# Kernel tuning notes

Hardware: AMD Instinct MI355X
Metric: run time of the kernel (lower is better)

## Reference

```python
import jax, jax.numpy as jnp
import numpy as np

HIDDEN = 4544
NUM_HEADS = 71
HEAD_DIM = 64
ROPE_BASE = 10000.0


def _rope_cos_sin(seq_len, dim, dtype):
    inv_freq = 1.0 / (ROPE_BASE ** (jnp.arange(0, dim, 2, dtype=jnp.float32) / dim))
    t = jnp.arange(seq_len, dtype=jnp.float32)
    freqs = jnp.einsum('i,j->ij', t, inv_freq)            # [S, dim/2]
    emb = jnp.concatenate([freqs, freqs], axis=-1)        # [S, dim]
    return jnp.cos(emb).astype(dtype), jnp.sin(emb).astype(dtype)


def _rotate_half(x):
    half = x.shape[-1] // 2
    return jnp.concatenate([-x[..., half:], x[..., :half]], axis=-1)


def _apply_rope(x, cos, sin):
    # x: [..., S, hd]; cos/sin: [S, hd]
    return x * cos + _rotate_half(x) * sin


def setup_inputs() -> dict:
    key = jax.random.key(0)
    k1, k2, k3 = jax.random.split(key, 3)
    B, S = 1, 1024
    hidden_states = jax.random.normal(k1, (B, 1, S, HIDDEN), dtype=jnp.float32) * 0.02
    # additive causal mask (prefill)
    neg = jnp.triu(jnp.full((S, S), -1e9, dtype=jnp.float32), k=1)
    attention_mask = jnp.broadcast_to(neg[None, None], (B, 1, S, S))
    # fused QKV weight (already transposed for right-matmul): [H, (nh+2)*hd]
    qkv_w = jax.random.normal(k2, (HIDDEN, (NUM_HEADS + 2) * HEAD_DIM), dtype=jnp.float32) * 0.02
    dense_w = jax.random.normal(k3, (HIDDEN, HIDDEN), dtype=jnp.float32) * 0.02
    return {"hidden_states": hidden_states, "attention_mask": attention_mask,
            "qkv_w": qkv_w, "dense_w": dense_w}


def reference(hidden_states, attention_mask, qkv_w, dense_w):
    B, _, S, H = hidden_states.shape
    nh, hd = NUM_HEADS, HEAD_DIM
    x = hidden_states[:, 0]                               # [B, S, H]
    fused = jnp.einsum('bsh,hf->bsf', x, qkv_w)           # [B, S, (nh+2)*hd]
    fused = fused.reshape(B, S, nh + 2, hd)
    q = jnp.transpose(fused[:, :, :nh, :], (0, 2, 1, 3))  # [B, nh, S, hd]
    k = fused[:, :, nh, :]                                # [B, S, hd]  (single KV head, MQA)
    v = fused[:, :, nh + 1, :]                            # [B, S, hd]
    cos, sin = _rope_cos_sin(S, hd, q.dtype)
    q = _apply_rope(q, cos, sin)
    k = _apply_rope(k, cos, sin)
    scale = 1.0 / np.sqrt(hd).astype(np.float32)
    scores = jnp.einsum('bhsd,btd->bhst', q, k) * scale   # [B, nh, S, S]
    scores = scores + attention_mask                      # broadcast over heads
    probs = jax.nn.softmax(scores, axis=-1)
    ctx = jnp.einsum('bhst,btd->bhsd', probs, v)          # [B, nh, S, hd]
    ctx = jnp.transpose(ctx, (0, 2, 1, 3)).reshape(B, S, nh * hd)
    out = jnp.einsum('bsh,hg->bsg', ctx, dense_w)         # [B, S, H]
    return out[:, None]                                   # [B, 1, S, H]
```

## Files before the change

kernel.cpp:

```cpp
#include <hip/hip_runtime.h>

#define S_LEN 1024
#define HID   4544
#define NH    71
#define NQKV  4672

typedef __attribute__((ext_vector_type(4))) float f32x4;
typedef __attribute__((ext_vector_type(4))) unsigned short u16x4;
typedef __attribute__((ext_vector_type(8))) unsigned short u16x8;
typedef __attribute__((ext_vector_type(8))) __bf16 bf16x8;

__device__ __forceinline__ bf16x8 as_bf(u16x8 v) { return __builtin_bit_cast(bf16x8, v); }

__device__ __forceinline__ unsigned short f2bf(float f) {
    unsigned u = __builtin_bit_cast(unsigned, f);
    return (unsigned short)((u + 0x7FFFu + ((u >> 16) & 1u)) >> 16);
}
__device__ __forceinline__ float bf2f(unsigned short u) {
    return __builtin_bit_cast(float, (unsigned)u << 16);
}
__device__ __forceinline__ unsigned pk2(float a, float b) {
    return (unsigned)f2bf(a) | ((unsigned)f2bf(b) << 16);
}
__device__ __forceinline__ void gload16(const void* g, void* l) {
    __builtin_amdgcn_global_load_lds((const __attribute__((address_space(1))) unsigned int*)g,
                                     (__attribute__((address_space(3))) unsigned int*)l,
                                     16, 0, 0);
}

__global__ __launch_bounds__(256) void cvt_x_kernel(const float4* __restrict__ x,
                                                    ushort4* __restrict__ y) {
    int i = blockIdx.x * 256 + threadIdx.x;
    float4 v = x[i];
    ushort4 r;
    r.x = f2bf(v.x); r.y = f2bf(v.y); r.z = f2bf(v.z); r.w = f2bf(v.w);
    y[i] = r;
}

__global__ __launch_bounds__(256) void cvt_wT_kernel(const float* __restrict__ w,
                                                     unsigned short* __restrict__ wt,
                                                     int K, int N) {
    __shared__ float t[64][65];
    int n0 = blockIdx.x * 64, k0 = blockIdx.y * 64;
    int tx = threadIdx.x & 15, ty = threadIdx.x >> 4;
#pragma unroll
    for (int r = 0; r < 64; r += 16) {
        int k = k0 + ty + r;
        float4 v = *(const float4*)&w[(size_t)k * N + n0 + tx * 4];
        t[ty + r][tx * 4 + 0] = v.x;
        t[ty + r][tx * 4 + 1] = v.y;
        t[ty + r][tx * 4 + 2] = v.z;
        t[ty + r][tx * 4 + 3] = v.w;
    }
    __syncthreads();
    int nr = threadIdx.x >> 2;
    int kq = (threadIdx.x & 3) * 16;
    unsigned short tmp[16];
#pragma unroll
    for (int z = 0; z < 16; z++) tmp[z] = f2bf(t[kq + z][nr]);
    u16x8* dst = (u16x8*)&wt[(size_t)(n0 + nr) * K + k0 + kq];
    dst[0] = *(const u16x8*)&tmp[0];
    dst[1] = *(const u16x8*)&tmp[8];
}

__global__ void rope_table_kernel(float* __restrict__ cs, float* __restrict__ sn) {
    int s = blockIdx.x, i = threadIdx.x;
    float inv = powf(10000.0f, -(2.0f * (float)i) / 64.0f);
    float f = (float)s * inv;
    cs[s * 32 + i] = cosf(f);
    sn[s * 32 + i] = sinf(f);
}

template<int EPI>
__global__ __launch_bounds__(256, 3) void gemm_bt_kernel(
        const unsigned short* __restrict__ A, const unsigned short* __restrict__ BT,
        void* __restrict__ Cout, const float* __restrict__ cs_t,
        const float* __restrict__ sn_t, unsigned short* __restrict__ k_out,
        unsigned short* __restrict__ v_out, int K, int ldc) {
    __shared__ unsigned short As[2][128 * 64];
    __shared__ unsigned short Bs[2][64 * 64];
    int p = blockIdx.x;
    int per = gridDim.x >> 3;
    int l = (p & 7) * per + (p >> 3);
    int m0 = (l & 7) * 128, ni_b = l >> 3, n0 = ni_b * 64;
    int t = threadIdx.x;
    int wv = t >> 6, lane = t & 63, lr = lane & 15, lg = lane >> 4;
    int mw = wv * 32;
    int sw = lr & 7;
    int srow = t >> 3, sc16 = t & 7;

    f32x4 acc[2][4];
#pragma unroll
    for (int mi = 0; mi < 2; mi++)
#pragma unroll
        for (int ni = 0; ni < 4; ni++) acc[mi][ni] = (f32x4)0.0f;

    const char* Ab = (const char*)A;
    const char* Bb = (const char*)BT;
    size_t rs = (size_t)K * 2;

    auto stage = [&](int step, int buf) {
        size_t kb = (size_t)step * 128;
#pragma unroll
        for (int i = 0; i < 4; i++) {
            int row = i * 32 + srow;
            int csrc = sc16 ^ (row & 7);
            gload16(Ab + (size_t)(m0 + row) * rs + kb + csrc * 16,
                    (char*)As[buf] + (i * 256 + t) * 16);
        }
#pragma unroll
        for (int i = 0; i < 2; i++) {
            int row = i * 32 + srow;
            int csrc = sc16 ^ (row & 7);
            gload16(Bb + (size_t)(n0 + row) * rs + kb + csrc * 16,
                    (char*)Bs[buf] + (i * 256 + t) * 16);
        }
    };

    int nsteps = K >> 6;
    stage(0, 0);
    if (nsteps > 1) stage(1, 1);
    for (int s = 0; s < nsteps; ++s) {
        int cur = s & 1;
        if (s + 1 < nsteps) { asm volatile("s_waitcnt vmcnt(4)" ::: "memory"); }
        else                { asm volatile("s_waitcnt vmcnt(0)" ::: "memory"); }
        __builtin_amdgcn_s_barrier();
        bf16x8 af[2][2], bfr[4][2];
#pragma unroll
        for (int mi = 0; mi < 2; mi++)
#pragma unroll
            for (int kk = 0; kk < 2; kk++) {
                int row = mw + mi * 16 + lr;
                af[mi][kk] = as_bf(*(const u16x8*)&As[cur][row * 64 + (((kk * 4 + lg) ^ sw) << 3)]);
            }
#pragma unroll
        for (int ni = 0; ni < 4; ni++)
#pragma unroll
            for (int kk = 0; kk < 2; kk++) {
                int row = ni * 16 + lr;
                bfr[ni][kk] = as_bf(*(const u16x8*)&Bs[cur][row * 64 + (((kk * 4 + lg) ^ sw) << 3)]);
            }
#pragma unroll
        for (int mi = 0; mi < 2; mi++)
#pragma unroll
            for (int ni = 0; ni < 4; ni++) {
                acc[mi][ni] = __builtin_amdgcn_mfma_f32_16x16x32_bf16(af[mi][0], bfr[ni][0], acc[mi][ni], 0, 0, 0);
                acc[mi][ni] = __builtin_amdgcn_mfma_f32_16x16x32_bf16(af[mi][1], bfr[ni][1], acc[mi][ni], 0, 0, 0);
            }
        __builtin_amdgcn_s_barrier();
        if (s + 2 < nsteps) stage(s + 2, cur);
    }

    if (EPI == 0) {
        float* C = (float*)Cout;
#pragma unroll
        for (int mi = 0; mi < 2; mi++)
#pragma unroll
            for (int ni = 0; ni < 4; ni++) {
                int col = n0 + ni * 16 + lr;
#pragma unroll
                for (int i = 0; i < 4; i++) {
                    int row = m0 + mw + mi * 16 + 4 * lg + i;
                    C[(size_t)row * ldc + col] = acc[mi][ni][i];
                }
            }
    } else {
        int hh = ni_b;
        if (hh == 72) {
#pragma unroll
            for (int mi = 0; mi < 2; mi++)
#pragma unroll
                for (int ni = 0; ni < 4; ni++) {
                    int d = ni * 16 + lr;
                    int s0 = m0 + mw + mi * 16 + 4 * lg;
                    u16x4 pk;
#pragma unroll
                    for (int i = 0; i < 4; i++) pk[i] = f2bf(acc[mi][ni][i]);
                    *(u16x4*)&v_out[(size_t)d * S_LEN + s0] = pk;
                }
        } else {
            unsigned short* qb = (unsigned short*)Cout;
            float qscale = (hh < 71) ? 0.125f : 1.0f;
#pragma unroll
            for (int mi = 0; mi < 2; mi++)
#pragma unroll
                for (int i = 0; i < 4; i++) {
                    int s = m0 + mw + mi * 16 + 4 * lg + i;
                    float c0 = cs_t[s * 32 + lr],      g0 = sn_t[s * 32 + lr];
                    float c1 = cs_t[s * 32 + 16 + lr], g1 = sn_t[s * 32 + 16 + lr];
#pragma unroll
                    for (int ni = 0; ni < 4; ni++) {
                        float x  = acc[mi][ni][i];
                        float xp = acc[mi][ni ^ 2][i];
                        float c = (ni & 1) ? c1 : c0;
                        float g = (ni & 1) ? g1 : g0;
                        float r = (ni < 2) ? (x * c - xp * g) : (x * c + xp * g);
                        r *= qscale;
                        int d = ni * 16 + lr;
                        if (hh < 71) qb[(size_t)s * HID + hh * 64 + d] = f2bf(r);
                        else         k_out[(size_t)s * 64 + d] = f2bf(r);
                    }
                }
        }
    }
}

__global__ __launch_bounds__(256, 3) void attn_kernel(
        const unsigned short* __restrict__ qb, const unsigned short* __restrict__ kr,
        const unsigned short* __restrict__ vt, unsigned short* __restrict__ ctx,
        unsigned short* __restrict__ Opart, float2* __restrict__ MLpart) {
    __shared__ unsigned short Ks[2][64 * 64];
    __shared__ unsigned short Vs[2][64 * 64];
    __shared__ unsigned short Pl[4][16 * 72];
    int h = blockIdx.y;
    int u = blockIdx.x;
    int c, j0;
    if (u < 16)      { c = 0; j0 = u * 4; }
    else if (u < 28) { c = 1; j0 = 16 + (u - 16) * 4; }
    else if (u < 36) { c = 2; j0 = 32 + (u - 28) * 4; }
    else             { c = 3; j0 = 48 + (u - 36) * 4; }
    int t = threadIdx.x, wv = t >> 6, lane = t & 63, lr = lane & 15, lg = lane >> 4;
    int j = j0 + wv;
    int qs = j * 16 + lr;
    int k_lo = c * 256;
    int kend_w   = min((j + 1) * 16, k_lo + 256);
    int kend_max = min((j0 + 4) * 16, k_lo + 256);
    int nt = (kend_max - k_lo) >> 6;
    int nch = (j >> 4) + 1;
    int srow = t >> 3, sc16 = t & 7, sw = lr & 7;

    auto stage = [&](int ti, int buf) {
        size_t kbase = (size_t)(k_lo + ti * 64);
#pragma unroll
        for (int i = 0; i < 2; i++) {
            int row = i * 32 + srow;
            int csrc = sc16 ^ (row & 7);
            gload16((const char*)kr + (kbase + row) * 128 + csrc * 16,
                    (char*)Ks[buf] + (i * 256 + t) * 16);
        }
#pragma unroll
        for (int i = 0; i < 2; i++) {
            int row = i * 32 + srow;
            int csrc = sc16 ^ (row & 7);
            gload16((const char*)vt + (size_t)row * 2048 + kbase * 2 + csrc * 16,
                    (char*)Vs[buf] + (i * 256 + t) * 16);
        }
    };

    bf16x8 qf[2];
#pragma unroll
    for (int dc = 0; dc < 2; dc++)
        qf[dc] = as_bf(*(const u16x8*)&qb[(size_t)qs * HID + h * 64 + dc * 32 + 8 * lg]);

    float m_i = -1e30f, l_i = 0.0f;
    f32x4 o[4];
#pragma unroll
    for (int d4 = 0; d4 < 4; d4++) o[d4] = (f32x4)0.0f;

    stage(0, 0);
    if (nt > 1) stage(1, 1);

    for (int ti = 0; ti < nt; ti++) {
        int cur = ti & 1;
        if (ti + 1 < nt) { asm volatile("s_waitcnt vmcnt(4)" ::: "memory"); }
        else             { asm volatile("s_waitcnt vmcnt(0)" ::: "memory"); }
        __builtin_amdgcn_s_barrier();
        int k0 = k_lo + ti * 64;
        if (k0 < kend_w) {
            f32x4 st[4];
#pragma unroll
            for (int nc = 0; nc < 4; nc++) st[nc] = (f32x4)0.0f;
#pragma unroll
            for (int nc = 0; nc < 4; nc++) {
                int krow = nc * 16 + lr;
#pragma unroll
                for (int dc = 0; dc < 2; dc++) {
                    bf16x8 kf = as_bf(*(const u16x8*)&Ks[cur][krow * 64 + (((dc * 4 + lg) ^ sw) << 3)]);
                    st[nc] = __builtin_amdgcn_mfma_f32_16x16x32_bf16(kf, qf[dc], st[nc], 0, 0, 0);
                }
            }
            bool needmask = (k0 + 64 > j * 16);
            float mx = -1e30f;
            if (needmask) {
#pragma unroll
                for (int nc = 0; nc < 4; nc++)
#pragma unroll
                    for (int i = 0; i < 4; i++) {
                        int ks = k0 + nc * 16 + 4 * lg + i;
                        float v = (ks <= qs) ? st[nc][i] : -1e30f;
                        st[nc][i] = v;
                        mx = fmaxf(mx, v);
                    }
            } else {
#pragma unroll
                for (int nc = 0; nc < 4; nc++)
#pragma unroll
                    for (int i = 0; i < 4; i++) mx = fmaxf(mx, st[nc][i]);
            }
            mx = fmaxf(mx, __shfl_xor(mx, 16));
            mx = fmaxf(mx, __shfl_xor(mx, 32));
            if (!__all(mx <= m_i + 8.0f)) {
                float mn = fmaxf(m_i, mx);
                float so = __expf(m_i - mn);
                l_i *= so;
#pragma unroll
                for (int d4 = 0; d4 < 4; d4++)
#pragma unroll
                    for (int i = 0; i < 4; i++) o[d4][i] *= so;
                m_i = mn;
            }
            float ps = 0.0f;
#pragma unroll
            for (int nc = 0; nc < 4; nc++)
#pragma unroll
                for (int i = 0; i < 4; i++) {
                    float v = st[nc][i];
                    float e = (!needmask || v > -1e29f) ? __expf(v - m_i) : 0.0f;
                    st[nc][i] = e;
                    ps += e;
                }
            ps += __shfl_xor(ps, 16);
            ps += __shfl_xor(ps, 32);
            l_i += ps;
#pragma unroll
            for (int nc = 0; nc < 4; nc++) {
                *(unsigned*)&Pl[wv][lr * 72 + nc * 16 + 4 * lg]     = pk2(st[nc][0], st[nc][1]);
                *(unsigned*)&Pl[wv][lr * 72 + nc * 16 + 4 * lg + 2] = pk2(st[nc][2], st[nc][3]);
            }
            bf16x8 pb[2];
#pragma unroll
            for (int kk = 0; kk < 2; kk++)
                pb[kk] = as_bf(*(const u16x8*)&Pl[wv][lr * 72 + kk * 32 + 8 * lg]);
#pragma unroll
            for (int d4 = 0; d4 < 4; d4++) {
                int vrow = d4 * 16 + lr;
#pragma unroll
                for (int kk = 0; kk < 2; kk++) {
                    bf16x8 vf = as_bf(*(const u16x8*)&Vs[cur][vrow * 64 + (((kk * 4 + lg) ^ sw) << 3)]);
                    o[d4] = __builtin_amdgcn_mfma_f32_16x16x32_bf16(vf, pb[kk], o[d4], 0, 0, 0);
                }
            }
        }
        __builtin_amdgcn_s_barrier();
        if (ti + 2 < nt) stage(ti + 2, cur);
    }

    if (nch == 1) {
        float linv = 1.0f / l_i;
#pragma unroll
        for (int d4 = 0; d4 < 4; d4++) {
            u16x4 pk;
#pragma unroll
            for (int i = 0; i < 4; i++) pk[i] = f2bf(o[d4][i] * linv);
            *(u16x4*)&ctx[(size_t)qs * HID + h * 64 + d4 * 16 + 4 * lg] = pk;
        }
    } else {
        int pi = (h * 48 + (j - 16)) * 4 + c;
#pragma unroll
        for (int d4 = 0; d4 < 4; d4++) {
            u16x4 pk;
#pragma unroll
            for (int i = 0; i < 4; i++) pk[i] = f2bf(o[d4][i]);
            *(u16x4*)&Opart[(size_t)pi * 1024 + lr * 64 + d4 * 16 + 4 * lg] = pk;
        }
        if (lg == 0) MLpart[pi * 16 + lr] = make_float2(m_i, l_i);
    }
}

__global__ __launch_bounds__(256) void merge_kernel(
        const unsigned short* __restrict__ Opart, const float2* __restrict__ MLpart,
        unsigned short* __restrict__ ctx) {
    int mu = blockIdx.x * 4 + (threadIdx.x >> 6);
    int lane = threadIdx.x & 63;
    int h = mu / 48, jj = mu % 48, j = 16 + jj;
    int nch = (j >> 4) + 1;
    int base = (h * 48 + jj) * 4;
    for (int q = 0; q < 16; q++) {
        float m[4], l[4], w[4];
        float M = -1e30f;
        for (int c = 0; c < nch; c++) {
            float2 ml = MLpart[(base + c) * 16 + q];
            m[c] = ml.x; l[c] = ml.y;
            M = fmaxf(M, m[c]);
        }
        float L = 0.0f;
        for (int c = 0; c < nch; c++) { w[c] = __expf(m[c] - M); L += l[c] * w[c]; }
        float acc = 0.0f;
        for (int c = 0; c < nch; c++)
            acc += w[c] * bf2f(Opart[(size_t)(base + c) * 1024 + q * 64 + lane]);
        ctx[(size_t)(j * 16 + q) * HID + h * 64 + lane] = f2bf(acc / L);
    }
}

extern "C" void kernel_launch(void* const* d_in, const int* in_sizes, int n_in,
                              void* d_out, int out_size, void* d_ws, size_t ws_size,
                              hipStream_t stream) {
    const float* hs      = (const float*)d_in[0];
    const float* qkv_w   = (const float*)d_in[2];
    const float* dense_w = (const float*)d_in[3];
    float* out = (float*)d_out;

    char* ws = (char*)d_ws;
    size_t off = 0;
    auto alloc = [&](size_t bytes) -> void* {
        void* p = ws + off;
        off += (bytes + 255) & ~(size_t)255;
        return p;
    };
    unsigned short* x_bf   = (unsigned short*)alloc((size_t)S_LEN * HID * 2);
    unsigned short* wqkvT  = (unsigned short*)alloc((size_t)NQKV * HID * 2);
    unsigned short* q_bf   = (unsigned short*)alloc((size_t)S_LEN * HID * 2);
    unsigned short* k_rope = (unsigned short*)alloc((size_t)S_LEN * 64 * 2);
    unsigned short* v_t    = (unsigned short*)alloc((size_t)64 * S_LEN * 2);
    unsigned short* ctx    = (unsigned short*)alloc((size_t)S_LEN * HID * 2);
    unsigned short* wdT    = (unsigned short*)alloc((size_t)HID * HID * 2);
    float*          cs_t   = (float*)alloc((size_t)S_LEN * 32 * 4);
    float*          sn_t   = (float*)alloc((size_t)S_LEN * 32 * 4);
    (void)ws_size;
    unsigned short* Opart  = wqkvT;
    float2*         MLpart = (float2*)((char*)wqkvT + (size_t)71 * 48 * 4 * 1024 * 2);

    cvt_x_kernel<<<dim3(S_LEN * HID / 1024), dim3(256), 0, stream>>>(
        (const float4*)hs, (ushort4*)x_bf);
    cvt_wT_kernel<<<dim3(NQKV / 64, HID / 64), dim3(256), 0, stream>>>(
        qkv_w, wqkvT, HID, NQKV);
    cvt_wT_kernel<<<dim3(HID / 64, HID / 64), dim3(256), 0, stream>>>(
        dense_w, wdT, HID, HID);
    rope_table_kernel<<<dim3(S_LEN), dim3(32), 0, stream>>>(cs_t, sn_t);

    gemm_bt_kernel<1><<<dim3(NQKV / 64 * 8), dim3(256), 0, stream>>>(
        x_bf, wqkvT, q_bf, cs_t, sn_t, k_rope, v_t, HID, HID);

    attn_kernel<<<dim3(40, NH), dim3(256), 0, stream>>>(
        q_bf, k_rope, v_t, ctx, Opart, MLpart);

    merge_kernel<<<dim3(NH * 48 / 4), dim3(256), 0, stream>>>(Opart, MLpart, ctx);

    gemm_bt_kernel<0><<<dim3(HID / 64 * 8), dim3(256), 0, stream>>>(
        ctx, wdT, out, nullptr, nullptr, nullptr, nullptr, HID, HID);
}
```

Before: 251.5 us.

## Switch GEMM to 32x32x16 MFMA with two-wave 64x64 warp tiles

The bf16 GEMM kernel moves from 4 waves with 32x64 per-wave tiles of 16x16x32 MFMAs to 2 waves (128 threads), each computing a 64x64 tile with 32x32x16 MFMAs. LDS fragments are read into registers before the second barrier so the next stage's global-to-LDS prefetch can be issued ahead of the MFMA loop. The epilogues, including fused RoPE and V transpose, are remapped to the 32x32 accumulator layout. This aims for fewer LDS reads per FLOP and better MFMA throughput, at the cost of fewer waves per block, higher register pressure and less latency hiding.

```diff
diff --git a/kernel.cpp b/kernel.cpp
--- a/kernel.cpp
+++ b/kernel.cpp
@@ -5,7 +5,8 @@
 #define NH    71
 #define NQKV  4672
 
-typedef __attribute__((ext_vector_type(4))) float f32x4;
+typedef __attribute__((ext_vector_type(4)))  float f32x4;
+typedef __attribute__((ext_vector_type(16))) float f32x16;
 typedef __attribute__((ext_vector_type(4))) unsigned short u16x4;
 typedef __attribute__((ext_vector_type(8))) unsigned short u16x8;
 typedef __attribute__((ext_vector_type(8))) __bf16 bf16x8;
@@ -72,7 +73,7 @@
 }
 
 template<int EPI>
-__global__ __launch_bounds__(256, 3) void gemm_bt_kernel(
+__global__ __launch_bounds__(128, 2) void gemm_bt_kernel(
         const unsigned short* __restrict__ A, const unsigned short* __restrict__ BT,
         void* __restrict__ Cout, const float* __restrict__ cs_t,
         const float* __restrict__ sn_t, unsigned short* __restrict__ k_out,
@@ -84,16 +85,16 @@
     int l = (p & 7) * per + (p >> 3);
     int m0 = (l & 7) * 128, ni_b = l >> 3, n0 = ni_b * 64;
     int t = threadIdx.x;
-    int wv = t >> 6, lane = t & 63, lr = lane & 15, lg = lane >> 4;
-    int mw = wv * 32;
-    int sw = lr & 7;
-    int srow = t >> 3, sc16 = t & 7;
-
-    f32x4 acc[2][4];
+    int wv = t >> 6, lane = t & 63;
+    int lrow = lane & 31;
+    int lk   = lane >> 5;
+    int mw = wv * 64;
+
+    f32x16 acc[2][2];
 #pragma unroll
     for (int mi = 0; mi < 2; mi++)
 #pragma unroll
-        for (int ni = 0; ni < 4; ni++) acc[mi][ni] = (f32x4)0.0f;
+        for (int ni = 0; ni < 2; ni++) acc[mi][ni] = (f32x16)0.0f;
 
     const char* Ab = (const char*)A;
     const char* Bb = (const char*)BT;
@@ -102,18 +103,20 @@
     auto stage = [&](int step, int buf) {
         size_t kb = (size_t)step * 128;
 #pragma unroll
+        for (int i = 0; i < 8; i++) {
+            int chunk = i * 128 + t;
+            int row = chunk >> 3, c16 = chunk & 7;
+            int csrc = c16 ^ (row & 7);
+            gload16(Ab + (size_t)(m0 + row) * rs + kb + csrc * 16,
+                    (char*)As[buf] + chunk * 16);
+        }
+#pragma unroll
         for (int i = 0; i < 4; i++) {
-            int row = i * 32 + srow;
-            int csrc = sc16 ^ (row & 7);
-            gload16(Ab + (size_t)(m0 + row) * rs + kb + csrc * 16,
-                    (char*)As[buf] + (i * 256 + t) * 16);
-        }
-#pragma unroll
-        for (int i = 0; i < 2; i++) {
-            int row = i * 32 + srow;
-            int csrc = sc16 ^ (row & 7);
+            int chunk = i * 128 + t;
+            int row = chunk >> 3, c16 = chunk & 7;
+            int csrc = c16 ^ (row & 7);
             gload16(Bb + (size_t)(n0 + row) * rs + kb + csrc * 16,
-                    (char*)Bs[buf] + (i * 256 + t) * 16);
+                    (char*)Bs[buf] + chunk * 16);
         }
     };
 
@@ -122,33 +125,35 @@
     if (nsteps > 1) stage(1, 1);
     for (int s = 0; s < nsteps; ++s) {
         int cur = s & 1;
-        if (s + 1 < nsteps) { asm volatile("s_waitcnt vmcnt(4)" ::: "memory"); }
+        if (s + 1 < nsteps) { asm volatile("s_waitcnt vmcnt(12)" ::: "memory"); }
         else                { asm volatile("s_waitcnt vmcnt(0)" ::: "memory"); }
         __builtin_amdgcn_s_barrier();
-        bf16x8 af[2][2], bfr[4][2];
-#pragma unroll
-        for (int mi = 0; mi < 2; mi++)
-#pragma unroll
-            for (int kk = 0; kk < 2; kk++) {
-                int row = mw + mi * 16 + lr;
-                af[mi][kk] = as_bf(*(const u16x8*)&As[cur][row * 64 + (((kk * 4 + lg) ^ sw) << 3)]);
-            }
-#pragma unroll
-        for (int ni = 0; ni < 4; ni++)
-#pragma unroll
-            for (int kk = 0; kk < 2; kk++) {
-                int row = ni * 16 + lr;
-                bfr[ni][kk] = as_bf(*(const u16x8*)&Bs[cur][row * 64 + (((kk * 4 + lg) ^ sw) << 3)]);
-            }
-#pragma unroll
-        for (int mi = 0; mi < 2; mi++)
-#pragma unroll
-            for (int ni = 0; ni < 4; ni++) {
-                acc[mi][ni] = __builtin_amdgcn_mfma_f32_16x16x32_bf16(af[mi][0], bfr[ni][0], acc[mi][ni], 0, 0, 0);
-                acc[mi][ni] = __builtin_amdgcn_mfma_f32_16x16x32_bf16(af[mi][1], bfr[ni][1], acc[mi][ni], 0, 0, 0);
-            }
+        bf16x8 af[2][4], bfr[2][4];
+#pragma unroll
+        for (int mi = 0; mi < 2; mi++) {
+            int row = mw + mi * 32 + lrow;
+#pragma unroll
+            for (int kk = 0; kk < 4; kk++)
+                af[mi][kk] = as_bf(*(const u16x8*)&As[cur][row * 64 + (((kk * 2 + lk) ^ (row & 7)) << 3)]);
+        }
+#pragma unroll
+        for (int ni = 0; ni < 2; ni++) {
+            int row = ni * 32 + lrow;
+#pragma unroll
+            for (int kk = 0; kk < 4; kk++)
+                bfr[ni][kk] = as_bf(*(const u16x8*)&Bs[cur][row * 64 + (((kk * 2 + lk) ^ (row & 7)) << 3)]);
+        }
+        asm volatile("s_waitcnt lgkmcnt(0)" ::: "memory");
         __builtin_amdgcn_s_barrier();
         if (s + 2 < nsteps) stage(s + 2, cur);
+#pragma unroll
+        for (int kk = 0; kk < 4; kk++)
+#pragma unroll
+            for (int mi = 0; mi < 2; mi++)
+#pragma unroll
+                for (int ni = 0; ni < 2; ni++)
+                    acc[mi][ni] = __builtin_amdgcn_mfma_f32_32x32x16_bf16(
+                        af[mi][kk], bfr[ni][kk], acc[mi][ni], 0, 0, 0);
     }
 
     if (EPI == 0) {
@@ -156,12 +161,12 @@
 #pragma unroll
         for (int mi = 0; mi < 2; mi++)
 #pragma unroll
-            for (int ni = 0; ni < 4; ni++) {
-                int col = n0 + ni * 16 + lr;
-#pragma unroll
-                for (int i = 0; i < 4; i++) {
-                    int row = m0 + mw + mi * 16 + 4 * lg + i;
-                    C[(size_t)row * ldc + col] = acc[mi][ni][i];
+            for (int ni = 0; ni < 2; ni++) {
+                int col = n0 + ni * 32 + lrow;
+#pragma unroll
+                for (int r = 0; r < 16; r++) {
+                    int row = m0 + mw + mi * 32 + (r & 3) + 8 * (r >> 2) + 4 * lk;
+                    C[(size_t)row * ldc + col] = acc[mi][ni][r];
                 }
             }
     } else {
@@ -170,13 +175,16 @@
 #pragma unroll
             for (int mi = 0; mi < 2; mi++)
 #pragma unroll
-                for (int ni = 0; ni < 4; ni++) {
-                    int d = ni * 16 + lr;
-                    int s0 = m0 + mw + mi * 16 + 4 * lg;
-                    u16x4 pk;
-#pragma unroll
-                    for (int i = 0; i < 4; i++) pk[i] = f2bf(acc[mi][ni][i]);
-                    *(u16x4*)&v_out[(size_t)d * S_LEN + s0] = pk;
+                for (int ni = 0; ni < 2; ni++) {
+                    int d = ni * 32 + lrow;
+#pragma unroll
+                    for (int g = 0; g < 4; g++) {
+                        int s0 = m0 + mw + mi * 32 + 8 * g + 4 * lk;
+                        u16x4 pk;
+#pragma unroll
+                        for (int i = 0; i < 4; i++) pk[i] = f2bf(acc[mi][ni][g * 4 + i]);
+                        *(u16x4*)&v_out[(size_t)d * S_LEN + s0] = pk;
+                    }
                 }
         } else {
             unsigned short* qb = (unsigned short*)Cout;
@@ -184,21 +192,20 @@
 #pragma unroll
             for (int mi = 0; mi < 2; mi++)
 #pragma unroll
-                for (int i = 0; i < 4; i++) {
-                    int s = m0 + mw + mi * 16 + 4 * lg + i;
-                    float c0 = cs_t[s * 32 + lr],      g0 = sn_t[s * 32 + lr];
-                    float c1 = cs_t[s * 32 + 16 + lr], g1 = sn_t[s * 32 + 16 + lr];
-#pragma unroll
-                    for (int ni = 0; ni < 4; ni++) {
-                        float x  = acc[mi][ni][i];
-                        float xp = acc[mi][ni ^ 2][i];
-                        float c = (ni & 1) ? c1 : c0;
-                        float g = (ni & 1) ? g1 : g0;
-                        float r = (ni < 2) ? (x * c - xp * g) : (x * c + xp * g);
-                        r *= qscale;
-                        int d = ni * 16 + lr;
-                        if (hh < 71) qb[(size_t)s * HID + hh * 64 + d] = f2bf(r);
-                        else         k_out[(size_t)s * 64 + d] = f2bf(r);
+                for (int r = 0; r < 16; r++) {
+                    int s = m0 + mw + mi * 32 + (r & 3) + 8 * (r >> 2) + 4 * lk;
+                    float c = cs_t[s * 32 + lrow];
+                    float g = sn_t[s * 32 + lrow];
+                    float x0 = acc[mi][0][r];
+                    float x1 = acc[mi][1][r];
+                    float r0 = (x0 * c - x1 * g) * qscale;
+                    float r1 = (x1 * c + x0 * g) * qscale;
+                    if (hh < 71) {
+                        qb[(size_t)s * HID + hh * 64 + lrow]      = f2bf(r0);
+                        qb[(size_t)s * HID + hh * 64 + 32 + lrow] = f2bf(r1);
+                    } else {
+                        k_out[(size_t)s * 64 + lrow]      = f2bf(r0);
+                        k_out[(size_t)s * 64 + 32 + lrow] = f2bf(r1);
                     }
                 }
         }
@@ -428,7 +435,7 @@
         dense_w, wdT, HID, HID);
     rope_table_kernel<<<dim3(S_LEN), dim3(32), 0, stream>>>(cs_t, sn_t);
 
-    gemm_bt_kernel<1><<<dim3(NQKV / 64 * 8), dim3(256), 0, stream>>>(
+    gemm_bt_kernel<1><<<dim3(NQKV / 64 * 8), dim3(128), 0, stream>>>(
         x_bf, wqkvT, q_bf, cs_t, sn_t, k_rope, v_t, HID, HID);
 
     attn_kernel<<<dim3(40, NH), dim3(256), 0, stream>>>(
@@ -436,6 +443,6 @@
 
     merge_kernel<<<dim3(NH * 48 / 4), dim3(256), 0, stream>>>(Opart, MLpart, ctx);
 
-    gemm_bt_kernel<0><<<dim3(HID / 64 * 8), dim3(256), 0, stream>>>(
+    gemm_bt_kernel<0><<<dim3(HID / 64 * 8), dim3(128), 0, stream>>>(
         ctx, wdT, out, nullptr, nullptr, nullptr, nullptr, HID, HID);
 }
```

Measured after the change: 296.4 us. 17.9% more time.

## Retile GEMMs to 64x128 blocks with two waves and padded weights

Applied to the files above, without the earlier changes.

The GEMM tile changes from 128x64 with four waves to 64x128 with two waves, each wave computing a 64x64 sub-tile. The N dimension of the weights is padded (4736 and 4608) so it divides into 128-wide tiles, and stores are guarded by n_store. MFMAs are now issued after the barrier and after the next stage's prefetch, to overlap loads with compute and raise per-wave register reuse. The risks are fewer waves per block, lower occupancy and a smaller grid, plus extra padded work in the weight conversion.

```diff
diff --git a/kernel.cpp b/kernel.cpp
--- a/kernel.cpp
+++ b/kernel.cpp
@@ -4,8 +4,10 @@
 #define HID   4544
 #define NH    71
 #define NQKV  4672
-
-typedef __attribute__((ext_vector_type(4))) float f32x4;
+#define NQKV_PAD 4736
+#define ND_PAD   4608
+
+typedef __attribute__((ext_vector_type(4)))  float f32x4;
 typedef __attribute__((ext_vector_type(4))) unsigned short u16x4;
 typedef __attribute__((ext_vector_type(8))) unsigned short u16x8;
 typedef __attribute__((ext_vector_type(8))) __bf16 bf16x8;
@@ -46,7 +48,9 @@
 #pragma unroll
     for (int r = 0; r < 64; r += 16) {
         int k = k0 + ty + r;
-        float4 v = *(const float4*)&w[(size_t)k * N + n0 + tx * 4];
+        int n = n0 + tx * 4;
+        float4 v = make_float4(0.f, 0.f, 0.f, 0.f);
+        if (n < N) v = *(const float4*)&w[(size_t)k * N + n];
         t[ty + r][tx * 4 + 0] = v.x;
         t[ty + r][tx * 4 + 1] = v.y;
         t[ty + r][tx * 4 + 2] = v.z;
@@ -72,26 +76,25 @@
 }
 
 template<int EPI>
-__global__ __launch_bounds__(256, 3) void gemm_bt_kernel(
+__global__ __launch_bounds__(128, 2) void gemm_bt_kernel(
         const unsigned short* __restrict__ A, const unsigned short* __restrict__ BT,
         void* __restrict__ Cout, const float* __restrict__ cs_t,
         const float* __restrict__ sn_t, unsigned short* __restrict__ k_out,
-        unsigned short* __restrict__ v_out, int K, int ldc) {
-    __shared__ unsigned short As[2][128 * 64];
-    __shared__ unsigned short Bs[2][64 * 64];
+        unsigned short* __restrict__ v_out, int K, int ldc, int n_store) {
+    __shared__ unsigned short As[2][64 * 64];
+    __shared__ unsigned short Bs[2][128 * 64];
     int p = blockIdx.x;
     int per = gridDim.x >> 3;
     int l = (p & 7) * per + (p >> 3);
-    int m0 = (l & 7) * 128, ni_b = l >> 3, n0 = ni_b * 64;
+    int msl = l & 15, nb = l >> 4;
+    int m0 = msl * 64, n0 = nb * 128;
     int t = threadIdx.x;
-    int wv = t >> 6, lane = t & 63, lr = lane & 15, lg = lane >> 4;
-    int mw = wv * 32;
-    int sw = lr & 7;
-    int srow = t >> 3, sc16 = t & 7;
-
-    f32x4 acc[2][4];
-#pragma unroll
-    for (int mi = 0; mi < 2; mi++)
+    int wn = t >> 6;
+    int lane = t & 63, lr = lane & 15, lg = lane >> 4;
+
+    f32x4 acc[4][4];
+#pragma unroll
+    for (int mi = 0; mi < 4; mi++)
 #pragma unroll
         for (int ni = 0; ni < 4; ni++) acc[mi][ni] = (f32x4)0.0f;
 
@@ -103,17 +106,19 @@
         size_t kb = (size_t)step * 128;
 #pragma unroll
         for (int i = 0; i < 4; i++) {
-            int row = i * 32 + srow;
-            int csrc = sc16 ^ (row & 7);
+            int chunk = i * 128 + t;
+            int row = chunk >> 3, c8 = chunk & 7;
+            int csrc = c8 ^ (row & 7);
             gload16(Ab + (size_t)(m0 + row) * rs + kb + csrc * 16,
-                    (char*)As[buf] + (i * 256 + t) * 16);
-        }
-#pragma unroll
-        for (int i = 0; i < 2; i++) {
-            int row = i * 32 + srow;
-            int csrc = sc16 ^ (row & 7);
+                    (char*)As[buf] + chunk * 16);
+        }
+#pragma unroll
+        for (int i = 0; i < 8; i++) {
+            int chunk = i * 128 + t;
+            int row = chunk >> 3, c8 = chunk & 7;
+            int csrc = c8 ^ (row & 7);
             gload16(Bb + (size_t)(n0 + row) * rs + kb + csrc * 16,
-                    (char*)Bs[buf] + (i * 256 + t) * 16);
+                    (char*)Bs[buf] + chunk * 16);
         }
     };
 
@@ -122,70 +127,74 @@
     if (nsteps > 1) stage(1, 1);
     for (int s = 0; s < nsteps; ++s) {
         int cur = s & 1;
-        if (s + 1 < nsteps) { asm volatile("s_waitcnt vmcnt(4)" ::: "memory"); }
+        if (s + 1 < nsteps) { asm volatile("s_waitcnt vmcnt(12)" ::: "memory"); }
         else                { asm volatile("s_waitcnt vmcnt(0)" ::: "memory"); }
         __builtin_amdgcn_s_barrier();
-        bf16x8 af[2][2], bfr[4][2];
-#pragma unroll
-        for (int mi = 0; mi < 2; mi++)
-#pragma unroll
-            for (int kk = 0; kk < 2; kk++) {
-                int row = mw + mi * 16 + lr;
-                af[mi][kk] = as_bf(*(const u16x8*)&As[cur][row * 64 + (((kk * 4 + lg) ^ sw) << 3)]);
-            }
-#pragma unroll
-        for (int ni = 0; ni < 4; ni++)
-#pragma unroll
-            for (int kk = 0; kk < 2; kk++) {
-                int row = ni * 16 + lr;
-                bfr[ni][kk] = as_bf(*(const u16x8*)&Bs[cur][row * 64 + (((kk * 4 + lg) ^ sw) << 3)]);
-            }
-#pragma unroll
-        for (int mi = 0; mi < 2; mi++)
-#pragma unroll
-            for (int ni = 0; ni < 4; ni++) {
-                acc[mi][ni] = __builtin_amdgcn_mfma_f32_16x16x32_bf16(af[mi][0], bfr[ni][0], acc[mi][ni], 0, 0, 0);
-                acc[mi][ni] = __builtin_amdgcn_mfma_f32_16x16x32_bf16(af[mi][1], bfr[ni][1], acc[mi][ni], 0, 0, 0);
-            }
+        bf16x8 af[4][2], bfr[4][2];
+#pragma unroll
+        for (int mi = 0; mi < 4; mi++) {
+            int row = mi * 16 + lr;
+#pragma unroll
+            for (int kk = 0; kk < 2; kk++)
+                af[mi][kk] = as_bf(*(const u16x8*)&As[cur][row * 64 + (((kk * 4 + lg) ^ (row & 7)) << 3)]);
+        }
+#pragma unroll
+        for (int ni = 0; ni < 4; ni++) {
+            int row = wn * 64 + ni * 16 + lr;
+#pragma unroll
+            for (int kk = 0; kk < 2; kk++)
+                bfr[ni][kk] = as_bf(*(const u16x8*)&Bs[cur][row * 64 + (((kk * 4 + lg) ^ (row & 7)) << 3)]);
+        }
+        asm volatile("s_waitcnt lgkmcnt(0)" ::: "memory");
         __builtin_amdgcn_s_barrier();
         if (s + 2 < nsteps) stage(s + 2, cur);
+#pragma unroll
+        for (int kk = 0; kk < 2; kk++)
+#pragma unroll
+            for (int mi = 0; mi < 4; mi++)
+#pragma unroll
+                for (int ni = 0; ni < 4; ni++)
+                    acc[mi][ni] = __builtin_amdgcn_mfma_f32_16x16x32_bf16(
+                        af[mi][kk], bfr[ni][kk], acc[mi][ni], 0, 0, 0);
     }
 
     if (EPI == 0) {
         float* C = (float*)Cout;
 #pragma unroll
-        for (int mi = 0; mi < 2; mi++)
+        for (int mi = 0; mi < 4; mi++)
 #pragma unroll
             for (int ni = 0; ni < 4; ni++) {
-                int col = n0 + ni * 16 + lr;
-#pragma unroll
-                for (int i = 0; i < 4; i++) {
-                    int row = m0 + mw + mi * 16 + 4 * lg + i;
-                    C[(size_t)row * ldc + col] = acc[mi][ni][i];
+                int col = n0 + wn * 64 + ni * 16 + lr;
+                if (col < n_store) {
+#pragma unroll
+                    for (int i = 0; i < 4; i++) {
+                        int row = m0 + mi * 16 + 4 * lg + i;
+                        C[(size_t)row * ldc + col] = acc[mi][ni][i];
+                    }
                 }
             }
     } else {
-        int hh = ni_b;
+        int hh = nb * 2 + wn;
         if (hh == 72) {
 #pragma unroll
-            for (int mi = 0; mi < 2; mi++)
+            for (int mi = 0; mi < 4; mi++)
 #pragma unroll
                 for (int ni = 0; ni < 4; ni++) {
                     int d = ni * 16 + lr;
-                    int s0 = m0 + mw + mi * 16 + 4 * lg;
+                    int s0 = m0 + mi * 16 + 4 * lg;
                     u16x4 pk;
 #pragma unroll
                     for (int i = 0; i < 4; i++) pk[i] = f2bf(acc[mi][ni][i]);
                     *(u16x4*)&v_out[(size_t)d * S_LEN + s0] = pk;
                 }
-        } else {
+        } else if (hh < 72) {
             unsigned short* qb = (unsigned short*)Cout;
             float qscale = (hh < 71) ? 0.125f : 1.0f;
 #pragma unroll
-            for (int mi = 0; mi < 2; mi++)
+            for (int mi = 0; mi < 4; mi++)
 #pragma unroll
                 for (int i = 0; i < 4; i++) {
-                    int s = m0 + mw + mi * 16 + 4 * lg + i;
+                    int s = m0 + mi * 16 + 4 * lg + i;
                     float c0 = cs_t[s * 32 + lr],      g0 = sn_t[s * 32 + lr];
                     float c1 = cs_t[s * 32 + 16 + lr], g1 = sn_t[s * 32 + 16 + lr];
 #pragma unroll
@@ -408,12 +417,12 @@
         return p;
     };
     unsigned short* x_bf   = (unsigned short*)alloc((size_t)S_LEN * HID * 2);
-    unsigned short* wqkvT  = (unsigned short*)alloc((size_t)NQKV * HID * 2);
+    unsigned short* wqkvT  = (unsigned short*)alloc((size_t)NQKV_PAD * HID * 2);
     unsigned short* q_bf   = (unsigned short*)alloc((size_t)S_LEN * HID * 2);
     unsigned short* k_rope = (unsigned short*)alloc((size_t)S_LEN * 64 * 2);
     unsigned short* v_t    = (unsigned short*)alloc((size_t)64 * S_LEN * 2);
     unsigned short* ctx    = (unsigned short*)alloc((size_t)S_LEN * HID * 2);
-    unsigned short* wdT    = (unsigned short*)alloc((size_t)HID * HID * 2);
+    unsigned short* wdT    = (unsigned short*)alloc((size_t)ND_PAD * HID * 2);
     float*          cs_t   = (float*)alloc((size_t)S_LEN * 32 * 4);
     float*          sn_t   = (float*)alloc((size_t)S_LEN * 32 * 4);
     (void)ws_size;
@@ -422,20 +431,20 @@
 
     cvt_x_kernel<<<dim3(S_LEN * HID / 1024), dim3(256), 0, stream>>>(
         (const float4*)hs, (ushort4*)x_bf);
-    cvt_wT_kernel<<<dim3(NQKV / 64, HID / 64), dim3(256), 0, stream>>>(
+    cvt_wT_kernel<<<dim3(NQKV_PAD / 64, HID / 64), dim3(256), 0, stream>>>(
         qkv_w, wqkvT, HID, NQKV);
-    cvt_wT_kernel<<<dim3(HID / 64, HID / 64), dim3(256), 0, stream>>>(
+    cvt_wT_kernel<<<dim3(ND_PAD / 64, HID / 64), dim3(256), 0, stream>>>(
         dense_w, wdT, HID, HID);
     rope_table_kernel<<<dim3(S_LEN), dim3(32), 0, stream>>>(cs_t, sn_t);
 
-    gemm_bt_kernel<1><<<dim3(NQKV / 64 * 8), dim3(256), 0, stream>>>(
-        x_bf, wqkvT, q_bf, cs_t, sn_t, k_rope, v_t, HID, HID);
+    gemm_bt_kernel<1><<<dim3(16 * NQKV_PAD / 128), dim3(128), 0, stream>>>(
+        x_bf, wqkvT, q_bf, cs_t, sn_t, k_rope, v_t, HID, HID, NQKV);
 
     attn_kernel<<<dim3(40, NH), dim3(256), 0, stream>>>(
         q_bf, k_rope, v_t, ctx, Opart, MLpart);
 
     merge_kernel<<<dim3(NH * 48 / 4), dim3(256), 0, stream>>>(Opart, MLpart, ctx);
 
-    gemm_bt_kernel<0><<<dim3(HID / 64 * 8), dim3(256), 0, stream>>>(
-        ctx, wdT, out, nullptr, nullptr, nullptr, nullptr, HID, HID);
-}
+    gemm_bt_kernel<0><<<dim3(16 * ND_PAD / 128), dim3(128), 0, stream>>>(
+        ctx, wdT, out, nullptr, nullptr, nullptr, nullptr, HID, HID, HID);
+}
```

Result: slower. 259.2 us (+3.0%).
